# Kernel tuning notes

Hardware: AMD Instinct MI355X
Metric: run time of the kernel (lower is better)

The kernel has to match this reference:

```python
import jax, jax.numpy as jnp
import numpy as np

B, S, D = 4, 2048, 1024

def setup_inputs() -> dict:
    key = jax.random.key(0)
    ks = jax.random.split(key, 9)
    q = jax.random.normal(ks[0], (B, S, D), dtype=jnp.float32)
    k = jax.random.normal(ks[1], (B, S, D), dtype=jnp.float32)
    v = jax.random.normal(ks[2], (B, S, D), dtype=jnp.float32)
    # Dense layer params (Glorot-ish scale), bias included like keras Dense
    sc = 1.0 / np.sqrt(D)
    Wq = jax.random.normal(ks[3], (D, D), dtype=jnp.float32) * sc
    Wk = jax.random.normal(ks[4], (D, D), dtype=jnp.float32) * sc
    Wv = jax.random.normal(ks[5], (D, D), dtype=jnp.float32) * sc
    bq = jnp.zeros((D,), dtype=jnp.float32)
    bk = jnp.zeros((D,), dtype=jnp.float32)
    bv = jnp.zeros((D,), dtype=jnp.float32)
    # causal mask: 1 where attention is forbidden (future positions)
    mask = jnp.triu(jnp.ones((S, S), dtype=jnp.float32), k=1)
    return {"q": q, "k": k, "v": v, "mask": mask,
            "Wq": Wq, "bq": bq, "Wk": Wk, "bk": bk, "Wv": Wv, "bv": bv}

def reference(q, k, v, mask, Wq, bq, Wk, bk, Wv, bv):
    WQ = q @ Wq + bq                      # [B,S,D]
    WK = k @ Wk + bk
    WV = v @ Wv + bv
    d_k = jnp.asarray(WK.shape[-1], dtype=jnp.float32)
    scores = jnp.einsum('bqd,bkd->bqk', WQ, WK) / jnp.sqrt(d_k)  # [B,S,S]
    scores = scores + mask * (-1e9)
    attn = jax.nn.softmax(scores, axis=-1)
    return jnp.einsum('bqk,bkd->bqd', attn, WV)
```

## Files before the change

### kernel.cpp

```cpp
#include <hip/hip_runtime.h>
#include <math.h>

#define S_LEN 2048
#define D_DIM 1024
#define NB    4

typedef __bf16 bf16_t;
typedef __bf16 bf16x8 __attribute__((ext_vector_type(8)));
typedef float  f32x4  __attribute__((ext_vector_type(4)));
typedef unsigned int   u32;
typedef unsigned short u16;
typedef unsigned int   u32x4 __attribute__((ext_vector_type(4)));

#define BM 128
#define BN 128
#define BK 64

__device__ __forceinline__ u16 f2b_bits(float x) {
    bf16_t h = (bf16_t)x;
    return *(u16*)&h;
}

__device__ __forceinline__ void async16(const void* g, void* l) {
    __builtin_amdgcn_global_load_lds(
        (__attribute__((address_space(1))) const void*)g,
        (__attribute__((address_space(3))) void*)l, 16, 0, 0);
}

__device__ __forceinline__ void gemm_bt_core(
    const bf16_t* __restrict__ A, const bf16_t* __restrict__ Bt,
    int lda, int ldb, int m0, int n0, int kTiles, f32x4 (&acc)[4][4])
{
    __shared__ bf16_t lA[BM * BK];
    __shared__ bf16_t lB[BN * BK];
    const int t    = threadIdx.x;
    const int w    = t >> 6;
    const int lane = t & 63;
    const int wr   = w >> 1, wc = w & 1;
    const int srow   = lane >> 3;
    const int kb_src = ((lane & 7) ^ (lane >> 3)) * 8;
    const int fr = lane & 15, fq = lane >> 4;
    const int fof0 = (((0 * 4 + fq) ^ (fr & 7)) * 8);
    const int fof1 = (((1 * 4 + fq) ^ (fr & 7)) * 8);
    const bf16_t* paB0 = lA + (wr * 64 + fr) * BK + fof0;
    const bf16_t* paB1 = lA + (wr * 64 + fr) * BK + fof1;
    const bf16_t* pbB0 = lB + (wc * 64 + fr) * BK + fof0;
    const bf16_t* pbB1 = lB + (wc * 64 + fr) * BK + fof1;
    bf16_t* ldsA = lA + (w * 32) * BK;
    bf16_t* ldsB = lB + (w * 32) * BK;
    const bf16_t* gA = A  + (long)(m0 + w * 32 + srow) * lda + kb_src;
    const bf16_t* gB = Bt + (long)(n0 + w * 32 + srow) * ldb + kb_src;

#pragma unroll
    for (int mt = 0; mt < 4; ++mt)
#pragma unroll
        for (int nt = 0; nt < 4; ++nt)
            acc[mt][nt] = f32x4{0.f, 0.f, 0.f, 0.f};

    for (int kt = 0; kt < kTiles; ++kt) {
        const long k0 = (long)kt * BK;
#pragma unroll
        for (int i = 0; i < 4; ++i) {
            async16(gA + k0 + (long)(i * 8) * lda, ldsA + i * 8 * BK);
            async16(gB + k0 + (long)(i * 8) * ldb, ldsB + i * 8 * BK);
        }
        asm volatile("s_waitcnt vmcnt(0)" ::: "memory");
        __syncthreads();
#pragma unroll
        for (int h = 0; h < 2; ++h) {
            const bf16_t* pa = h ? paB1 : paB0;
            const bf16_t* pb = h ? pbB1 : pbB0;
            bf16x8 af[4], bfv[4];
#pragma unroll
            for (int mt = 0; mt < 4; ++mt)
                af[mt] = *(const bf16x8*)(pa + mt * 16 * BK);
#pragma unroll
            for (int nt = 0; nt < 4; ++nt)
                bfv[nt] = *(const bf16x8*)(pb + nt * 16 * BK);
#pragma unroll
            for (int mt = 0; mt < 4; ++mt)
#pragma unroll
                for (int nt = 0; nt < 4; ++nt)
                    acc[mt][nt] = __builtin_amdgcn_mfma_f32_16x16x32_bf16(
                        af[mt], bfv[nt], acc[mt][nt], 0, 0, 0);
        }
        __syncthreads();
    }
}

__global__ __launch_bounds__(256) void k_f2b(
    const float* __restrict__ q, const float* __restrict__ k,
    const float* __restrict__ v, bf16_t* __restrict__ Xb)
{
    const int z = blockIdx.z;
    const float* src = (z == 0) ? q : ((z == 1) ? k : v);
    bf16_t* dst = Xb + (long)z * ((long)NB * S_LEN * D_DIM);
    const long i = (long)blockIdx.x * blockDim.x + threadIdx.x;
    float4 a = ((const float4*)src)[i];
    u32 lo = (u32)f2b_bits(a.x) | ((u32)f2b_bits(a.y) << 16);
    u32 hi = (u32)f2b_bits(a.z) | ((u32)f2b_bits(a.w) << 16);
    ((uint2*)(dst))[i] = make_uint2(lo, hi);
}

__global__ __launch_bounds__(256) void k_tw(
    const float* __restrict__ Wq, const float* __restrict__ Wk,
    const float* __restrict__ Wv, bf16_t* __restrict__ Wt)
{
    __shared__ u32 tile[64][33];
    const int z = blockIdx.z;
    const float* W = (z == 0) ? Wq : ((z == 1) ? Wk : Wv);
    bf16_t* T = Wt + (long)z * D_DIM * D_DIM;
    const int t = threadIdx.x;
    const int k0 = blockIdx.x * 64, n0 = blockIdx.y * 64;
#pragma unroll
    for (int rr = 0; rr < 4; ++rr) {
        const int kr = (t >> 4) + rr * 16;
        const int nq = (t & 15) * 4;
        float4 f = *(const float4*)(W + (long)(k0 + kr) * D_DIM + n0 + nq);
        tile[kr][(nq >> 1)]     = (u32)f2b_bits(f.x) | ((u32)f2b_bits(f.y) << 16);
        tile[kr][(nq >> 1) + 1] = (u32)f2b_bits(f.z) | ((u32)f2b_bits(f.w) << 16);
    }
    __syncthreads();
#pragma unroll
    for (int rr = 0; rr < 2; ++rr) {
        const int nr = (t >> 3) + rr * 32;
        const int j0 = (t & 7) * 4;
        u32x4 o;
#pragma unroll
        for (int jj = 0; jj < 4; ++jj) {
            const int j = j0 + jj;
            const u32 ua = tile[2 * j][nr >> 1];
            const u32 ub = tile[2 * j + 1][nr >> 1];
            const u32 lo = (nr & 1) ? (ua >> 16) : (ua & 0xffffu);
            const u32 hi = (nr & 1) ? (ub >> 16) : (ub & 0xffffu);
            o[jj] = lo | (hi << 16);
        }
        *(u32x4*)(T + (long)(n0 + nr) * D_DIM + k0 + 2 * j0) = o;
    }
}

__global__ __launch_bounds__(256) void k_tv(
    const bf16_t* __restrict__ PrV, bf16_t* __restrict__ WVt)
{
    __shared__ u32 tile[64][33];
    const int b = blockIdx.z;
    const bf16_t* src = PrV + (long)b * S_LEN * D_DIM;
    bf16_t* dst = WVt + (long)b * D_DIM * S_LEN;
    const int t = threadIdx.x;
    const int d0 = blockIdx.x * 64, s0 = blockIdx.y * 64;
#pragma unroll
    for (int rr = 0; rr < 2; ++rr) {
        const int sr = (t >> 3) + rr * 32;
        const int dp0 = (t & 7) * 4;
        u32x4 u = *(const u32x4*)(src + (long)(s0 + sr) * D_DIM + d0 + 2 * dp0);
#pragma unroll
        for (int q = 0; q < 4; ++q) tile[sr][dp0 + q] = u[q];
    }
    __syncthreads();
#pragma unroll
    for (int rr = 0; rr < 2; ++rr) {
        const int dr = (t >> 3) + rr * 32;
        const int j0 = (t & 7) * 4;
        u32x4 o;
#pragma unroll
        for (int jj = 0; jj < 4; ++jj) {
            const int j = j0 + jj;
            const u32 ua = tile[2 * j][dr >> 1];
            const u32 ub = tile[2 * j + 1][dr >> 1];
            const u32 lo = (dr & 1) ? (ua >> 16) : (ua & 0xffffu);
            const u32 hi = (dr & 1) ? (ub >> 16) : (ub & 0xffffu);
            o[jj] = lo | (hi << 16);
        }
        *(u32x4*)(dst + (long)(d0 + dr) * S_LEN + s0 + 2 * j0) = o;
    }
}

__global__ __launch_bounds__(256) void k_gemm_proj(
    const bf16_t* __restrict__ Xb, const bf16_t* __restrict__ Wt,
    const float* __restrict__ bq, const float* __restrict__ bk,
    const float* __restrict__ bv, bf16_t* __restrict__ Pr)
{
    const int z = blockIdx.z;
    const bf16_t* A  = Xb + (long)z * ((long)NB * S_LEN * D_DIM);
    const bf16_t* Bt = Wt + (long)z * D_DIM * D_DIM;
    bf16_t* C        = Pr + (long)z * ((long)NB * S_LEN * D_DIM);
    const float* bias = (z == 0) ? bq : ((z == 1) ? bk : bv);
    const int m0 = blockIdx.x * BM, n0 = blockIdx.y * BN;
    f32x4 acc[4][4];
    gemm_bt_core(A, Bt, D_DIM, D_DIM, m0, n0, D_DIM / BK, acc);
    const int lane = threadIdx.x & 63, w = threadIdx.x >> 6;
    const int wr = w >> 1, wc = w & 1;
    const int r0 = m0 + wr * 64 + (lane >> 4) * 4;
    const int c0 = n0 + wc * 64 + (lane & 15);
#pragma unroll
    for (int mt = 0; mt < 4; ++mt)
#pragma unroll
        for (int nt = 0; nt < 4; ++nt) {
            const int col = c0 + nt * 16;
            const float bb = bias[col];
#pragma unroll
            for (int r = 0; r < 4; ++r) {
                const int row = r0 + mt * 16 + r;
                C[(long)row * D_DIM + col] = (bf16_t)(acc[mt][nt][r] + bb);
            }
        }
}

__global__ __launch_bounds__(256) void k_gemm_scores(
    const bf16_t* __restrict__ PrQ, const bf16_t* __restrict__ PrK,
    bf16_t* __restrict__ SC)
{
    const int u = blockIdx.x, b = blockIdx.z;
    int ti = (int)((sqrtf(8.0f * (float)u + 1.0f) - 1.0f) * 0.5f);
    while ((ti + 1) * (ti + 2) / 2 <= u) ++ti;
    while (ti * (ti + 1) / 2 > u) --ti;
    const int tj = u - ti * (ti + 1) / 2;
    const bf16_t* A  = PrQ + (long)b * S_LEN * D_DIM;
    const bf16_t* Bt = PrK + (long)b * S_LEN * D_DIM;
    bf16_t* C        = SC  + (long)b * S_LEN * S_LEN;
    const int m0 = ti * BM, n0 = tj * BN;
    f32x4 acc[4][4];
    gemm_bt_core(A, Bt, D_DIM, D_DIM, m0, n0, D_DIM / BK, acc);
    const int lane = threadIdx.x & 63, w = threadIdx.x >> 6;
    const int wr = w >> 1, wc = w & 1;
    const int r0 = m0 + wr * 64 + (lane >> 4) * 4;
    const int c0 = n0 + wc * 64 + (lane & 15);
#pragma unroll
    for (int mt = 0; mt < 4; ++mt)
#pragma unroll
        for (int nt = 0; nt < 4; ++nt) {
            const int col = c0 + nt * 16;
#pragma unroll
            for (int r = 0; r < 4; ++r) {
                const int row = r0 + mt * 16 + r;
                C[(long)row * S_LEN + col] = (bf16_t)(acc[mt][nt][r] * 0.03125f);
            }
        }
}

__global__ __launch_bounds__(256) void k_softmax(bf16_t* __restrict__ SC)
{
    const int w = threadIdx.x >> 6, lane = threadIdx.x & 63;
    const int i = blockIdx.x * 4 + w;
    const int b = blockIdx.y;
    bf16_t* row = SC + ((long)b * S_LEN + i) * S_LEN;
    const int n    = i + 1;
    const int jend = ((i >> 7) + 1) << 7;
    const int nch  = (jend + 511) >> 9;
    float x[4][8];
    float mx = -1e30f;
#pragma unroll
    for (int c = 0; c < 4; ++c) {
        if (c < nch) {
            bf16x8 vv = *(const bf16x8*)(row + c * 512 + lane * 8);
#pragma unroll
            for (int e = 0; e < 8; ++e) {
                const int j = c * 512 + lane * 8 + e;
                const float f = (j < n) ? (float)vv[e] : -1e30f;
                x[c][e] = f;
                mx = fmaxf(mx, f);
            }
        }
    }
#pragma unroll
    for (int d = 1; d < 64; d <<= 1) mx = fmaxf(mx, __shfl_xor(mx, d, 64));
    float sm = 0.f;
#pragma unroll
    for (int c = 0; c < 4; ++c) {
        if (c < nch) {
#pragma unroll
            for (int e = 0; e < 8; ++e) {
                const int j = c * 512 + lane * 8 + e;
                float p = (j < n) ? __expf(x[c][e] - mx) : 0.f;
                x[c][e] = p;
                sm += p;
            }
        }
    }
#pragma unroll
    for (int d = 1; d < 64; d <<= 1) sm += __shfl_xor(sm, d, 64);
    const float inv = 1.0f / sm;
#pragma unroll
    for (int c = 0; c < 4; ++c) {
        if (c < nch) {
            bf16x8 o;
#pragma unroll
            for (int e = 0; e < 8; ++e) o[e] = (bf16_t)(x[c][e] * inv);
            *(bf16x8*)(row + c * 512 + lane * 8) = o;
        }
    }
}

__global__ __launch_bounds__(256) void k_gemm_pv(
    const bf16_t* __restrict__ SC, const bf16_t* __restrict__ WVt,
    float* __restrict__ Out)
{
    const int ti = (S_LEN / BM - 1) - blockIdx.y, b = blockIdx.z;
    const bf16_t* A  = SC  + (long)b * S_LEN * S_LEN;
    const bf16_t* Bt = WVt + (long)b * D_DIM * S_LEN;
    float* C         = Out + (long)b * S_LEN * D_DIM;
    const int m0 = ti * BM, n0 = blockIdx.x * BN;
    f32x4 acc[4][4];
    gemm_bt_core(A, Bt, S_LEN, S_LEN, m0, n0, (ti + 1) * (BM / BK), acc);
    const int lane = threadIdx.x & 63, w = threadIdx.x >> 6;
    const int wr = w >> 1, wc = w & 1;
    const int r0 = m0 + wr * 64 + (lane >> 4) * 4;
    const int c0 = n0 + wc * 64 + (lane & 15);
#pragma unroll
    for (int mt = 0; mt < 4; ++mt)
#pragma unroll
        for (int nt = 0; nt < 4; ++nt) {
            const int col = c0 + nt * 16;
#pragma unroll
            for (int r = 0; r < 4; ++r) {
                const int row = r0 + mt * 16 + r;
                C[(long)row * D_DIM + col] = acc[mt][nt][r];
            }
        }
}

extern "C" void kernel_launch(void* const* d_in, const int* in_sizes, int n_in,
                              void* d_out, int out_size, void* d_ws, size_t ws_size,
                              hipStream_t stream)
{
    (void)in_sizes; (void)n_in; (void)out_size; (void)ws_size;
    const float* q  = (const float*)d_in[0];
    const float* k  = (const float*)d_in[1];
    const float* v  = (const float*)d_in[2];
    const float* Wq = (const float*)d_in[4];
    const float* bq = (const float*)d_in[5];
    const float* Wk = (const float*)d_in[6];
    const float* bk = (const float*)d_in[7];
    const float* Wv = (const float*)d_in[8];
    const float* bv = (const float*)d_in[9];
    float* out = (float*)d_out;

    bf16_t* ws = (bf16_t*)d_ws;
    const long nW = (long)D_DIM * D_DIM;
    const long nX = (long)NB * S_LEN * D_DIM;
    bf16_t* Wt  = ws;
    bf16_t* Xb  = Wt + 3 * nW;
    bf16_t* SC  = Xb;
    bf16_t* Pr  = Xb + 3 * nX;
    bf16_t* WVt = Pr + 3 * nX;
    bf16_t* PrQ = Pr;
    bf16_t* PrK = Pr + nX;
    bf16_t* PrV = Pr + 2 * nX;

    k_f2b        <<<dim3(8192, 1, 3),   256,        0, stream>>>(q, k, v, Xb);
    k_tw         <<<dim3(16, 16, 3),    256,        0, stream>>>(Wq, Wk, Wv, Wt);
    k_gemm_proj  <<<dim3(64, 8, 3),     256,        0, stream>>>(Xb, Wt, bq, bk, bv, Pr);
    k_tv         <<<dim3(16, 32, NB),   256,        0, stream>>>(PrV, WVt);
    k_gemm_scores<<<dim3(136, 1, NB),   256,        0, stream>>>(PrQ, PrK, SC);
    k_softmax    <<<dim3(S_LEN / 4, NB),256,        0, stream>>>(SC);
    k_gemm_pv    <<<dim3(8, 16, NB),    256,        0, stream>>>(SC, WVt, out);
}
```

Measured before the change: 315.2 us.

## Double-buffer LDS tiles in score and PV GEMMs with async prefetch

```diff
diff --git a/kernel.cpp b/kernel.cpp
--- a/kernel.cpp
+++ b/kernel.cpp
@@ -26,6 +26,8 @@
         (__attribute__((address_space(1))) const void*)g,
         (__attribute__((address_space(3))) void*)l, 16, 0, 0);
 }
+
+#define BAR_RAW() asm volatile("s_barrier" ::: "memory")
 
 __device__ __forceinline__ void gemm_bt_core(
     const bf16_t* __restrict__ A, const bf16_t* __restrict__ Bt,
@@ -88,6 +90,79 @@
     }
 }
 
+__device__ __forceinline__ void gemm_bt_dbuf(
+    const bf16_t* __restrict__ A, const bf16_t* __restrict__ Bt,
+    int lda, int ldb, int m0, int n0, int kTiles, f32x4 (&acc)[4][4])
+{
+    __shared__ bf16_t lA[2][BM * BK];
+    __shared__ bf16_t lB[2][BN * BK];
+    const int t    = threadIdx.x;
+    const int w    = t >> 6;
+    const int lane = t & 63;
+    const int wr   = w >> 1, wc = w & 1;
+    const int srow   = lane >> 3;
+    const int kb_src = ((lane & 7) ^ (lane >> 3)) * 8;
+    const int fr = lane & 15, fq = lane >> 4;
+    const int fof0 = (((0 * 4 + fq) ^ (fr & 7)) * 8);
+    const int fof1 = (((1 * 4 + fq) ^ (fr & 7)) * 8);
+    const int aO0 = (wr * 64 + fr) * BK + fof0;
+    const int aO1 = (wr * 64 + fr) * BK + fof1;
+    const int bO0 = (wc * 64 + fr) * BK + fof0;
+    const int bO1 = (wc * 64 + fr) * BK + fof1;
+    const int sOf = (w * 32) * BK;
+    const bf16_t* gA = A  + (long)(m0 + w * 32 + srow) * lda + kb_src;
+    const bf16_t* gB = Bt + (long)(n0 + w * 32 + srow) * ldb + kb_src;
+
+#pragma unroll
+    for (int mt = 0; mt < 4; ++mt)
+#pragma unroll
+        for (int nt = 0; nt < 4; ++nt)
+            acc[mt][nt] = f32x4{0.f, 0.f, 0.f, 0.f};
+
+#pragma unroll
+    for (int i = 0; i < 4; ++i) {
+        async16(gA + (long)(i * 8) * lda, &lA[0][sOf + i * 8 * BK]);
+        async16(gB + (long)(i * 8) * ldb, &lB[0][sOf + i * 8 * BK]);
+    }
+
+    for (int kt = 0; kt < kTiles; ++kt) {
+        const int cur = kt & 1, nxt = cur ^ 1;
+        if (kt + 1 < kTiles) {
+            const long k1 = (long)(kt + 1) * BK;
+#pragma unroll
+            for (int i = 0; i < 4; ++i) {
+                async16(gA + k1 + (long)(i * 8) * lda, &lA[nxt][sOf + i * 8 * BK]);
+                async16(gB + k1 + (long)(i * 8) * ldb, &lB[nxt][sOf + i * 8 * BK]);
+            }
+            asm volatile("s_waitcnt vmcnt(8)" ::: "memory");
+        } else {
+            asm volatile("s_waitcnt vmcnt(0)" ::: "memory");
+        }
+        BAR_RAW();
+        const bf16_t* lac = lA[cur];
+        const bf16_t* lbc = lB[cur];
+#pragma unroll
+        for (int h = 0; h < 2; ++h) {
+            const bf16_t* pa = lac + (h ? aO1 : aO0);
+            const bf16_t* pb = lbc + (h ? bO1 : bO0);
+            bf16x8 af[4], bfv[4];
+#pragma unroll
+            for (int mt = 0; mt < 4; ++mt)
+                af[mt] = *(const bf16x8*)(pa + mt * 16 * BK);
+#pragma unroll
+            for (int nt = 0; nt < 4; ++nt)
+                bfv[nt] = *(const bf16x8*)(pb + nt * 16 * BK);
+#pragma unroll
+            for (int mt = 0; mt < 4; ++mt)
+#pragma unroll
+                for (int nt = 0; nt < 4; ++nt)
+                    acc[mt][nt] = __builtin_amdgcn_mfma_f32_16x16x32_bf16(
+                        af[mt], bfv[nt], acc[mt][nt], 0, 0, 0);
+        }
+        BAR_RAW();
+    }
+}
+
 __global__ __launch_bounds__(256) void k_f2b(
     const float* __restrict__ q, const float* __restrict__ k,
     const float* __restrict__ v, bf16_t* __restrict__ Xb)
@@ -220,7 +295,7 @@
     bf16_t* C        = SC  + (long)b * S_LEN * S_LEN;
     const int m0 = ti * BM, n0 = tj * BN;
     f32x4 acc[4][4];
-    gemm_bt_core(A, Bt, D_DIM, D_DIM, m0, n0, D_DIM / BK, acc);
+    gemm_bt_dbuf(A, Bt, D_DIM, D_DIM, m0, n0, D_DIM / BK, acc);
     const int lane = threadIdx.x & 63, w = threadIdx.x >> 6;
     const int wr = w >> 1, wc = w & 1;
     const int r0 = m0 + wr * 64 + (lane >> 4) * 4;
@@ -301,7 +376,7 @@
     float* C         = Out + (long)b * S_LEN * D_DIM;
     const int m0 = ti * BM, n0 = blockIdx.x * BN;
     f32x4 acc[4][4];
-    gemm_bt_core(A, Bt, S_LEN, S_LEN, m0, n0, (ti + 1) * (BM / BK), acc);
+    gemm_bt_dbuf(A, Bt, S_LEN, S_LEN, m0, n0, (ti + 1) * (BM / BK), acc);
     const int lane = threadIdx.x & 63, w = threadIdx.x >> 6;
     const int wr = w >> 1, wc = w & 1;
     const int r0 = m0 + wr * 64 + (lane >> 4) * 4;
```

New measurement: 316.1 us. Within noise of the previous version (+0.3%).
